# Kernel optimization log

Hardware: AMD Instinct MI355X
Metric: run time of the kernel (lower is better)

## Reference

```python
import jax, jax.numpy as jnp
import numpy as np

B, T, D, L, E = 8, 2048, 256, 8, 64


def setup_inputs() -> dict:
    key = jax.random.key(0)
    ks = jax.random.split(key, 5)
    x = jax.random.normal(ks[0], (B, T, D), dtype=jnp.float32)
    # MMLP params: weight (4L, D, E), bias (4L, E); nn.Linear: (2L, D), (2L,)
    W_ml = jax.random.normal(ks[1], (4 * L, D, E), dtype=jnp.float32) * 0.05
    b_ml = jax.random.normal(ks[2], (4 * L, E), dtype=jnp.float32) * 0.05
    W_lin = jax.random.normal(ks[3], (2 * L, D), dtype=jnp.float32) * 0.05
    b_lin = jax.random.normal(ks[4], (2 * L,), dtype=jnp.float32) * 0.05
    return {"x": x, "W_ml": W_ml, "b_ml": b_ml, "W_lin": W_lin, "b_lin": b_lin}


def _xlstm_forward(x, W_ml, b_ml, W_lin, b_lin):
    b, t, _ = x.shape
    l4, _, e = W_ml.shape
    l = l4 // 4
    # Precompute all per-step gate projections at once (the torch code does this per step).
    mg = jnp.einsum('bti,lij->btlj', x, W_ml) + b_ml          # (B,T,4L,E)
    lg = jnp.einsum('bti,li->btl', x, W_lin) + b_lin          # (B,T,2L)
    o_, v, k, q = jnp.split(mg, 4, axis=2)                    # each (B,T,L,E)
    i_, f_ = jnp.split(lg, 2, axis=2)                         # each (B,T,L)
    xs = tuple(jnp.moveaxis(a, 1, 0) for a in (o_, v, k, q, i_, f_))  # time-major

    def step(carry, inp):
        m, n, C, h = carry
        o_t, v_t, k_t, q_t, i_t, f_t = inp
        m_new = jnp.maximum(f_t + m, i_t)                     # stabilizer (B,L)
        i_g = jnp.exp(i_t - m_new)
        f_g = jnp.exp(f_t + m - m_new)
        # rank-1 outer-product update of matrix cell state (B,L,E,E)
        C = f_g[:, :, None, None] * C + i_g[:, :, None, None] * (v_t[:, :, :, None] * k_t[:, :, None, :])
        n = f_g[:, :, None] * n + i_g[:, :, None] * k_t       # (B,L,E)
        denom = jnp.maximum(jnp.sum(n * q_t, axis=-1), 1.0)[:, :, None]  # clamp(.,1,inf)
        h = jax.nn.sigmoid(o_t) * jnp.einsum('blij,bli->blj', C, q_t) / denom
        return (m_new, n, C, h), None

    init = (
        jnp.zeros((b, l), jnp.float32),
        jnp.zeros((b, l, e), jnp.float32),
        jnp.zeros((b, l, e, e), jnp.float32),
        jnp.zeros((b, l, e), jnp.float32),
    )
    (m, n, C, h), _ = jax.lax.scan(step, init, xs)
    return h, C


def reference(x, W_ml, b_ml, W_lin, b_lin):
    return _xlstm_forward(x, W_ml, b_ml, W_lin, b_lin)
```

## Files before the change

### kernel.cpp

```cpp
#include <hip/hip_runtime.h>

#define B 8
#define T 2048
#define D 256
#define L 8
#define E 64
#define BT (B*T)

typedef _Float16 f16;
typedef f16 f16x8 __attribute__((ext_vector_type(8)));
typedef float f32x4 __attribute__((ext_vector_type(4)));

#define OFF_I   0
#define OFF_F   (OFF_I  + B*L*T)
#define OFF_W16 (OFF_F  + B*L*T)
#define OFF_X16 (OFF_W16 + B*L*T/2)
#define OFF_WT  (OFF_X16 + B*T*D/2)
#define OFF_VT  (OFF_WT + 16*E*D/2)
#define OFF_KT  (OFF_VT + B*L*E*T/2)
#define OFF_CP  (OFF_KT + B*L*E*T/2)

__global__ __launch_bounds__(256) void k_prep_x(const float* __restrict__ x,
                                                f16* __restrict__ x16) {
    int i = (blockIdx.x * 256 + threadIdx.x) * 8;
    float4 v0 = *(const float4*)(x + i);
    float4 v1 = *(const float4*)(x + i + 4);
    f16x8 o;
    o[0] = (f16)v0.x; o[1] = (f16)v0.y; o[2] = (f16)v0.z; o[3] = (f16)v0.w;
    o[4] = (f16)v1.x; o[5] = (f16)v1.y; o[6] = (f16)v1.z; o[7] = (f16)v1.w;
    *(f16x8*)(x16 + i) = o;
}

__global__ __launch_bounds__(256) void k_prep_w(const float* __restrict__ Wml,
                                                f16* __restrict__ Wt16) {
    __shared__ float ts[64][65];
    int tid = threadIdx.x;
    int vkrow = blockIdx.x;
    int wrow = 8 + vkrow;
    for (int dc = 0; dc < 4; ++dc) {
        int d0 = dc * 64;
        int r = tid >> 2, cq = (tid & 3) * 16;
        const float* src = Wml + ((size_t)wrow * D + d0 + r) * E + cq;
        #pragma unroll
        for (int j = 0; j < 16; j += 4) {
            float4 v = *(const float4*)(src + j);
            ts[r][cq + j] = v.x; ts[r][cq + j + 1] = v.y;
            ts[r][cq + j + 2] = v.z; ts[r][cq + j + 3] = v.w;
        }
        __syncthreads();
        int e = tid >> 2, dq = (tid & 3) * 16;
        f16* dst = Wt16 + ((size_t)vkrow * E + e) * D + d0 + dq;
        f16x8 o0, o1;
        #pragma unroll
        for (int j = 0; j < 8; ++j) {
            o0[j] = (f16)ts[dq + j][e];
            o1[j] = (f16)ts[dq + 8 + j][e];
        }
        *(f16x8*)dst = o0;
        *(f16x8*)(dst + 8) = o1;
        __syncthreads();
    }
}

__global__ __launch_bounds__(256) void k_ifproj(const float* __restrict__ x,
        const float* __restrict__ Wlin, const float* __restrict__ blin,
        float* __restrict__ ibuf, float* __restrict__ fbuf) {
    __shared__ float xs[32][260];
    __shared__ float ws[16][260];
    int tid = threadIdx.x;
    int t0 = blockIdx.x * 32;
    {
        int row = tid >> 3, q = tid & 7;
        const float* src = x + (size_t)(t0 + row) * D + q * 32;
        #pragma unroll
        for (int j = 0; j < 8; ++j) {
            float4 v = *(const float4*)(src + j * 4);
            *(float4*)&xs[row][q * 32 + j * 4] = v;
        }
    }
    {
        int row = tid >> 4, c0 = (tid & 15) * 16;
        const float* src = Wlin + row * D + c0;
        #pragma unroll
        for (int j = 0; j < 4; ++j) {
            float4 v = *(const float4*)(src + j * 4);
            *(float4*)&ws[row][c0 + j * 4] = v;
        }
    }
    __syncthreads();
    int tl = tid >> 4, g = tid & 15;
    float acc0 = 0.f, acc1 = 0.f;
    for (int i = 0; i < D; ++i) {
        float wv = ws[g][i];
        acc0 += xs[tl * 2 + 0][i] * wv;
        acc1 += xs[tl * 2 + 1][i] * wv;
    }
    float bias = blin[g];
    float acc[2] = {acc0 + bias, acc1 + bias};
    #pragma unroll
    for (int u = 0; u < 2; ++u) {
        int t = t0 + tl * 2 + u;
        int b = t >> 11, tt = t & 2047;
        if (g < 8) ibuf[(b * L + g) * T + tt] = acc[u];
        else       fbuf[(b * L + (g - 8)) * T + tt] = acc[u];
    }
}

__global__ __launch_bounds__(256) void k_scan(const float* __restrict__ ibuf,
        const float* __restrict__ fbuf, f16* __restrict__ w16) {
    __shared__ float part[256];
    __shared__ float red[256];
    int tid = threadIdx.x;
    int base = blockIdx.x * T;
    const float* fp = fbuf + base + tid * 8;
    const float* ip = ibuf + base + tid * 8;
    float4 fa = *(const float4*)fp;
    float4 fb = *(const float4*)(fp + 4);
    float4 ia = *(const float4*)ip;
    float4 ib = *(const float4*)(ip + 4);
    float f[8] = {fa.x, fa.y, fa.z, fa.w, fb.x, fb.y, fb.z, fb.w};
    float iv[8] = {ia.x, ia.y, ia.z, ia.w, ib.x, ib.y, ib.z, ib.w};
    float ls[8]; float run = 0.f;
    #pragma unroll
    for (int r = 0; r < 8; ++r) { run += f[r]; ls[r] = run; }
    part[tid] = run;
    __syncthreads();
    if (tid == 0) {
        float running = 0.f;
        for (int k = 0; k < 256; ++k) { float tmp = part[k]; part[k] = running; running += tmp; }
    }
    __syncthreads();
    float off = part[tid];
    float e[8]; float lmax = -1e30f;
    #pragma unroll
    for (int r = 0; r < 8; ++r) { e[r] = iv[r] - (off + ls[r]); lmax = fmaxf(lmax, e[r]); }
    red[tid] = lmax;
    __syncthreads();
    for (int s = 128; s > 0; s >>= 1) {
        if (tid < s) red[tid] = fmaxf(red[tid], red[tid + s]);
        __syncthreads();
    }
    float M = fmaxf(red[0], 0.0f);
    f16x8 wv8;
    #pragma unroll
    for (int r = 0; r < 8; ++r) wv8[r] = (f16)__expf(e[r] - M);
    *(f16x8*)(w16 + base + tid * 8) = wv8;
}

__global__ __launch_bounds__(256) void k_vkproj_mfma(const f16* __restrict__ x16,
        const f16* __restrict__ Wt16, const float* __restrict__ bml,
        f16* __restrict__ Vt, f16* __restrict__ Kt) {
    __shared__ char lds[24576];
    int tid = threadIdx.x;
    int bx = blockIdx.x, by = blockIdx.y;
    int l = by >> 1, vk = by & 1;
    int vkrow = vk * 8 + l;
    int t0 = bx * 128;
    const f16* xa = x16 + (size_t)t0 * D;
    const f16* wb = Wt16 + (size_t)vkrow * E * D;
    int wv = tid >> 6, lane = tid & 63;
    f32x4 acc[2][4] = {};
    for (int kc = 0; kc < 4; ++kc) {
        int k0 = kc * 64;
        #pragma unroll
        for (int q = 0; q < 4; ++q) {
            int idx = q * 256 + tid;
            int row = idx >> 3, c = idx & 7;
            f16x8 v = *(const f16x8*)(xa + row * D + k0 + c * 8);
            int ba = row * 128 + c * 16; ba ^= (row & 7) << 4;
            *(f16x8*)(lds + ba) = v;
        }
        #pragma unroll
        for (int q = 0; q < 2; ++q) {
            int idx = q * 256 + tid;
            int e = idx >> 3, c = idx & 7;
            f16x8 v = *(const f16x8*)(wb + e * D + k0 + c * 8);
            int ba = 16384 + e * 128 + c * 16; ba ^= (e & 7) << 4;
            *(f16x8*)(lds + ba) = v;
        }
        __syncthreads();
        #pragma unroll
        for (int kk = 0; kk < 2; ++kk) {
            int ko = kk * 32 + (lane >> 4) * 8;
            f16x8 a[2], bfr[4];
            #pragma unroll
            for (int fr = 0; fr < 2; ++fr) {
                int row = wv * 32 + fr * 16 + (lane & 15);
                int ba = row * 128 + ko * 2; ba ^= (row & 7) << 4;
                a[fr] = *(const f16x8*)(lds + ba);
            }
            #pragma unroll
            for (int fc = 0; fc < 4; ++fc) {
                int e = fc * 16 + (lane & 15);
                int ba = 16384 + e * 128 + ko * 2; ba ^= (e & 7) << 4;
                bfr[fc] = *(const f16x8*)(lds + ba);
            }
            #pragma unroll
            for (int fr = 0; fr < 2; ++fr)
                #pragma unroll
                for (int fc = 0; fc < 4; ++fc)
                    acc[fr][fc] = __builtin_amdgcn_mfma_f32_16x16x32_f16(
                        a[fr], bfr[fc], acc[fr][fc], 0, 0, 0);
        }
        __syncthreads();
    }
    const float* bp = bml + (size_t)(8 + vkrow) * E;
    #pragma unroll
    for (int fr = 0; fr < 2; ++fr) {
        #pragma unroll
        for (int fc = 0; fc < 4; ++fc) {
            int e = fc * 16 + (lane & 15);
            float bias = bp[e];
            int swz = (e & 7) << 4;
            #pragma unroll
            for (int r = 0; r < 4; r += 2) {
                int t = wv * 32 + fr * 16 + (lane >> 4) * 4 + r;
                union { f16 h[2]; unsigned u; } pk;
                pk.h[0] = (f16)(acc[fr][fc][r] + bias);
                pk.h[1] = (f16)(acc[fr][fc][r + 1] + bias);
                int ba = e * 256 + t * 2; ba ^= swz;
                *(unsigned*)(lds + ba) = pk.u;
            }
        }
    }
    __syncthreads();
    f16* obuf = vk ? Kt : Vt;
    int e = tid >> 2, tq = (tid & 3) * 32;
    int b = t0 >> 11, tin = t0 & 2047;
    f16* dst = obuf + (((size_t)(b * L + l) * E + e) * T) + tin + tq;
    int swz = (e & 7) << 4;
    #pragma unroll
    for (int c = 0; c < 4; ++c) {
        int ba = e * 256 + (tq + c * 8) * 2; ba ^= swz;
        f16x8 v = *(const f16x8*)(lds + ba);
        *(f16x8*)(dst + c * 8) = v;
    }
}

__global__ __launch_bounds__(256) void k_cgemm_mfma(const f16* __restrict__ Vt,
        const f16* __restrict__ Kt, const f16* __restrict__ w16,
        float* __restrict__ Cpart) {
    int tid = threadIdx.x;
    int bl = blockIdx.x, tc = blockIdx.y;
    int wv = tid >> 6, lane = tid & 63;
    const f16* vp = Vt + (size_t)bl * E * T;
    const f16* kp = Kt + (size_t)bl * E * T;
    const f16* wp = w16 + (size_t)bl * T;
    f32x4 acc[5][4] = {};
    int tbase = tc * 512 + wv * 128;
    for (int kc = 0; kc < 4; ++kc) {
        int tt = tbase + kc * 32 + (lane >> 4) * 8;
        f16x8 wfrag = *(const f16x8*)(wp + tt);
        f16x8 a[5], bfr[4];
        #pragma unroll
        for (int m = 0; m < 4; ++m) {
            int i = m * 16 + (lane & 15);
            f16x8 v = *(const f16x8*)(vp + (size_t)i * T + tt);
            a[m] = v * wfrag;
        }
        a[4] = wfrag;
        #pragma unroll
        for (int nn = 0; nn < 4; ++nn) {
            int j = nn * 16 + (lane & 15);
            bfr[nn] = *(const f16x8*)(kp + (size_t)j * T + tt);
        }
        #pragma unroll
        for (int m = 0; m < 5; ++m)
            #pragma unroll
            for (int nn = 0; nn < 4; ++nn)
                acc[m][nn] = __builtin_amdgcn_mfma_f32_16x16x32_f16(
                    a[m], bfr[nn], acc[m][nn], 0, 0, 0);
    }
    float* cp = Cpart + ((size_t)bl * 16 + tc * 4 + wv) * (65 * 64);
    #pragma unroll
    for (int m = 0; m < 4; ++m)
        #pragma unroll
        for (int nn = 0; nn < 4; ++nn)
            #pragma unroll
            for (int r = 0; r < 4; ++r) {
                int row = m * 16 + (lane >> 4) * 4 + r;
                cp[row * 64 + nn * 16 + (lane & 15)] = acc[m][nn][r];
            }
    if ((lane >> 4) == 0) {
        #pragma unroll
        for (int nn = 0; nn < 4; ++nn)
            cp[4096 + nn * 16 + (lane & 15)] = acc[4][nn][0];
    }
}

__global__ __launch_bounds__(256) void k_final(const float* __restrict__ x,
        const float* __restrict__ Wml, const float* __restrict__ bml,
        const float* __restrict__ Cpart, float* __restrict__ out) {
    __shared__ float Cs[E * E];
    __shared__ float xs[D];
    __shared__ float ns[E];
    __shared__ float os[E];
    __shared__ float qs[E];
    int tid = threadIdx.x;
    int bl = blockIdx.x; int b = bl >> 3, l = bl & 7;
    xs[tid] = x[((size_t)(b * T + (T - 1))) * D + tid];
    const float* cp = Cpart + (size_t)bl * 16 * (65 * 64);
    #pragma unroll
    for (int j = 0; j < 4; ++j) {
        int idx = tid * 16 + j * 4;
        float4 s = {0, 0, 0, 0};
        for (int p = 0; p < 16; ++p) {
            float4 v = *(const float4*)(cp + p * (65 * 64) + idx);
            s.x += v.x; s.y += v.y; s.z += v.z; s.w += v.w;
        }
        *(float4*)&Cs[idx] = s;
        *(float4*)(out + 4096 + (size_t)bl * (E * E) + idx) = s;
    }
    if (tid < 64) {
        float s = 0.f;
        for (int p = 0; p < 16; ++p) s += cp[p * (65 * 64) + 4096 + tid];
        ns[tid] = s;
    }
    __syncthreads();
    if (tid < 128) {
        int gate = tid >> 6, e = tid & 63;
        int wrow = gate ? (3 * L + l) : l;
        const float* wpp = Wml + (size_t)wrow * D * E + e;
        float s = 0.f;
        for (int kk = 0; kk < D; ++kk) s += xs[kk] * wpp[kk * E];
        s += bml[wrow * E + e];
        if (gate) qs[e] = s; else os[e] = s;
    }
    __syncthreads();
    if (tid < 64) {
        int j = tid;
        float hc = 0.f;
        for (int i2 = 0; i2 < E; ++i2) hc += Cs[i2 * E + j] * qs[i2];
        float nq = 0.f;
        for (int i2 = 0; i2 < E; ++i2) nq += ns[i2] * qs[i2];
        float denom = fmaxf(nq, 1.0f);
        float sg = 1.0f / (1.0f + __expf(-os[j]));
        out[bl * E + j] = sg * hc / denom;
    }
}

extern "C" void kernel_launch(void* const* d_in, const int* in_sizes, int n_in,
                              void* d_out, int out_size, void* d_ws, size_t ws_size,
                              hipStream_t stream) {
    const float* x    = (const float*)d_in[0];
    const float* Wml  = (const float*)d_in[1];
    const float* bml  = (const float*)d_in[2];
    const float* Wlin = (const float*)d_in[3];
    const float* blin = (const float*)d_in[4];
    float* out = (float*)d_out;
    float* ws = (float*)d_ws;
    float* ibuf  = ws + OFF_I;
    float* fbuf  = ws + OFF_F;
    f16*   w16   = (f16*)(ws + OFF_W16);
    f16*   x16   = (f16*)(ws + OFF_X16);
    f16*   Wt16  = (f16*)(ws + OFF_WT);
    f16*   Vt    = (f16*)(ws + OFF_VT);
    f16*   Kt    = (f16*)(ws + OFF_KT);
    float* Cpart = ws + OFF_CP;

    k_prep_x<<<BT * D / (256 * 8), 256, 0, stream>>>(x, x16);
    k_prep_w<<<16, 256, 0, stream>>>(Wml, Wt16);
    k_ifproj<<<BT / 32, 256, 0, stream>>>(x, Wlin, blin, ibuf, fbuf);
    k_scan<<<B * L, 256, 0, stream>>>(ibuf, fbuf, w16);
    k_vkproj_mfma<<<dim3(BT / 128, 16), 256, 0, stream>>>(x16, Wt16, bml, Vt, Kt);
    k_cgemm_mfma<<<dim3(B * L, 4), 256, 0, stream>>>(Vt, Kt, w16, Cpart);
    k_final<<<B * L, 256, 0, stream>>>(x, Wml, bml, Cpart, out);
}
```

Baseline: 74.37 us.

## Fuse prep kernels, convert x in-GEMM, merge V/K projection, reduce C partials in LDS

Merges the i/f projection and W transpose into one launch and drops the separate fp32-to-fp16 pass over x, converting x while loading tiles in the V/K projection GEMM instead. Each V/K block now computes both V and K for a layer (128 output columns), so x is read half as often. The C-GEMM reduces its four wave partials in shared memory before writing, which cuts partial-sum traffic and the final reduction from 16 to 4. The cost is fp32 x loads being re-read per layer block (8 times), and serialized LDS accumulation across waves.

```diff
diff --git a/kernel.cpp b/kernel.cpp
--- a/kernel.cpp
+++ b/kernel.cpp
@@ -14,95 +14,85 @@
 #define OFF_I   0
 #define OFF_F   (OFF_I  + B*L*T)
 #define OFF_W16 (OFF_F  + B*L*T)
-#define OFF_X16 (OFF_W16 + B*L*T/2)
-#define OFF_WT  (OFF_X16 + B*T*D/2)
+#define OFF_WT  (OFF_W16 + B*L*T/2)
 #define OFF_VT  (OFF_WT + 16*E*D/2)
 #define OFF_KT  (OFF_VT + B*L*E*T/2)
 #define OFF_CP  (OFF_KT + B*L*E*T/2)
 
-__global__ __launch_bounds__(256) void k_prep_x(const float* __restrict__ x,
-                                                f16* __restrict__ x16) {
-    int i = (blockIdx.x * 256 + threadIdx.x) * 8;
-    float4 v0 = *(const float4*)(x + i);
-    float4 v1 = *(const float4*)(x + i + 4);
-    f16x8 o;
-    o[0] = (f16)v0.x; o[1] = (f16)v0.y; o[2] = (f16)v0.z; o[3] = (f16)v0.w;
-    o[4] = (f16)v1.x; o[5] = (f16)v1.y; o[6] = (f16)v1.z; o[7] = (f16)v1.w;
-    *(f16x8*)(x16 + i) = o;
-}
-
-__global__ __launch_bounds__(256) void k_prep_w(const float* __restrict__ Wml,
-                                                f16* __restrict__ Wt16) {
-    __shared__ float ts[64][65];
-    int tid = threadIdx.x;
-    int vkrow = blockIdx.x;
-    int wrow = 8 + vkrow;
-    for (int dc = 0; dc < 4; ++dc) {
-        int d0 = dc * 64;
-        int r = tid >> 2, cq = (tid & 3) * 16;
-        const float* src = Wml + ((size_t)wrow * D + d0 + r) * E + cq;
-        #pragma unroll
-        for (int j = 0; j < 16; j += 4) {
-            float4 v = *(const float4*)(src + j);
-            ts[r][cq + j] = v.x; ts[r][cq + j + 1] = v.y;
-            ts[r][cq + j + 2] = v.z; ts[r][cq + j + 3] = v.w;
-        }
-        __syncthreads();
-        int e = tid >> 2, dq = (tid & 3) * 16;
-        f16* dst = Wt16 + ((size_t)vkrow * E + e) * D + d0 + dq;
-        f16x8 o0, o1;
-        #pragma unroll
-        for (int j = 0; j < 8; ++j) {
-            o0[j] = (f16)ts[dq + j][e];
-            o1[j] = (f16)ts[dq + 8 + j][e];
-        }
-        *(f16x8*)dst = o0;
-        *(f16x8*)(dst + 8) = o1;
-        __syncthreads();
-    }
-}
-
-__global__ __launch_bounds__(256) void k_ifproj(const float* __restrict__ x,
+__global__ __launch_bounds__(256) void k_prep(const float* __restrict__ x,
         const float* __restrict__ Wlin, const float* __restrict__ blin,
-        float* __restrict__ ibuf, float* __restrict__ fbuf) {
-    __shared__ float xs[32][260];
-    __shared__ float ws[16][260];
-    int tid = threadIdx.x;
-    int t0 = blockIdx.x * 32;
-    {
-        int row = tid >> 3, q = tid & 7;
-        const float* src = x + (size_t)(t0 + row) * D + q * 32;
-        #pragma unroll
-        for (int j = 0; j < 8; ++j) {
-            float4 v = *(const float4*)(src + j * 4);
-            *(float4*)&xs[row][q * 32 + j * 4] = v;
-        }
-    }
-    {
-        int row = tid >> 4, c0 = (tid & 15) * 16;
-        const float* src = Wlin + row * D + c0;
-        #pragma unroll
-        for (int j = 0; j < 4; ++j) {
-            float4 v = *(const float4*)(src + j * 4);
-            *(float4*)&ws[row][c0 + j * 4] = v;
-        }
-    }
-    __syncthreads();
-    int tl = tid >> 4, g = tid & 15;
-    float acc0 = 0.f, acc1 = 0.f;
-    for (int i = 0; i < D; ++i) {
-        float wv = ws[g][i];
-        acc0 += xs[tl * 2 + 0][i] * wv;
-        acc1 += xs[tl * 2 + 1][i] * wv;
-    }
-    float bias = blin[g];
-    float acc[2] = {acc0 + bias, acc1 + bias};
-    #pragma unroll
-    for (int u = 0; u < 2; ++u) {
-        int t = t0 + tl * 2 + u;
-        int b = t >> 11, tt = t & 2047;
-        if (g < 8) ibuf[(b * L + g) * T + tt] = acc[u];
-        else       fbuf[(b * L + (g - 8)) * T + tt] = acc[u];
+        const float* __restrict__ Wml,
+        float* __restrict__ ibuf, float* __restrict__ fbuf,
+        f16* __restrict__ Wt16) {
+    __shared__ __align__(16) char smem[49920];
+    int tid = threadIdx.x;
+    int bx = blockIdx.x;
+    if (bx < 512) {
+        float (*xs)[260] = (float(*)[260])smem;
+        float (*wsm)[260] = (float(*)[260])(smem + 33280);
+        int t0 = bx * 32;
+        {
+            int row = tid >> 3, q = tid & 7;
+            const float* src = x + (size_t)(t0 + row) * D + q * 32;
+            #pragma unroll
+            for (int j = 0; j < 8; ++j) {
+                float4 v = *(const float4*)(src + j * 4);
+                *(float4*)&xs[row][q * 32 + j * 4] = v;
+            }
+        }
+        {
+            int row = tid >> 4, c0 = (tid & 15) * 16;
+            const float* src = Wlin + row * D + c0;
+            #pragma unroll
+            for (int j = 0; j < 4; ++j) {
+                float4 v = *(const float4*)(src + j * 4);
+                *(float4*)&wsm[row][c0 + j * 4] = v;
+            }
+        }
+        __syncthreads();
+        int tl = tid >> 4, g = tid & 15;
+        float acc0 = 0.f, acc1 = 0.f;
+        for (int i = 0; i < D; ++i) {
+            float wv = wsm[g][i];
+            acc0 += xs[tl * 2 + 0][i] * wv;
+            acc1 += xs[tl * 2 + 1][i] * wv;
+        }
+        float bias = blin[g];
+        float acc[2] = {acc0 + bias, acc1 + bias};
+        #pragma unroll
+        for (int u = 0; u < 2; ++u) {
+            int t = t0 + tl * 2 + u;
+            int b = t >> 11, tt = t & 2047;
+            if (g < 8) ibuf[(b * L + g) * T + tt] = acc[u];
+            else       fbuf[(b * L + (g - 8)) * T + tt] = acc[u];
+        }
+    } else {
+        float (*ts)[65] = (float(*)[65])smem;
+        int vkrow = bx - 512;
+        int wrow = 8 + vkrow;
+        for (int dc = 0; dc < 4; ++dc) {
+            int d0 = dc * 64;
+            int r = tid >> 2, cq = (tid & 3) * 16;
+            const float* src = Wml + ((size_t)wrow * D + d0 + r) * E + cq;
+            #pragma unroll
+            for (int j = 0; j < 16; j += 4) {
+                float4 v = *(const float4*)(src + j);
+                ts[r][cq + j] = v.x; ts[r][cq + j + 1] = v.y;
+                ts[r][cq + j + 2] = v.z; ts[r][cq + j + 3] = v.w;
+            }
+            __syncthreads();
+            int e = tid >> 2, dq = (tid & 3) * 16;
+            f16* dst = Wt16 + ((size_t)vkrow * E + e) * D + d0 + dq;
+            f16x8 o0, o1;
+            #pragma unroll
+            for (int j = 0; j < 8; ++j) {
+                o0[j] = (f16)ts[dq + j][e];
+                o1[j] = (f16)ts[dq + 8 + j][e];
+            }
+            *(f16x8*)dst = o0;
+            *(f16x8*)(dst + 8) = o1;
+            __syncthreads();
+        }
     }
 }
 
@@ -147,99 +137,107 @@
     *(f16x8*)(w16 + base + tid * 8) = wv8;
 }
 
-__global__ __launch_bounds__(256) void k_vkproj_mfma(const f16* __restrict__ x16,
+__global__ __launch_bounds__(256) void k_vkproj2(const float* __restrict__ x,
         const f16* __restrict__ Wt16, const float* __restrict__ bml,
         f16* __restrict__ Vt, f16* __restrict__ Kt) {
-    __shared__ char lds[24576];
-    int tid = threadIdx.x;
-    int bx = blockIdx.x, by = blockIdx.y;
-    int l = by >> 1, vk = by & 1;
-    int vkrow = vk * 8 + l;
+    __shared__ __align__(16) char lds[32768];
+    int tid = threadIdx.x;
+    int bx = blockIdx.x, l = blockIdx.y;
     int t0 = bx * 128;
-    const f16* xa = x16 + (size_t)t0 * D;
-    const f16* wb = Wt16 + (size_t)vkrow * E * D;
+    const float* xa = x + (size_t)t0 * D;
+    const f16* wvp = Wt16 + (size_t)l * E * D;
+    const f16* wkp = Wt16 + (size_t)(8 + l) * E * D;
     int wv = tid >> 6, lane = tid & 63;
-    f32x4 acc[2][4] = {};
+    f32x4 acc[2][8] = {};
     for (int kc = 0; kc < 4; ++kc) {
         int k0 = kc * 64;
         #pragma unroll
         for (int q = 0; q < 4; ++q) {
             int idx = q * 256 + tid;
             int row = idx >> 3, c = idx & 7;
-            f16x8 v = *(const f16x8*)(xa + row * D + k0 + c * 8);
-            int ba = row * 128 + c * 16; ba ^= (row & 7) << 4;
-            *(f16x8*)(lds + ba) = v;
-        }
-        #pragma unroll
-        for (int q = 0; q < 2; ++q) {
+            const float* src = xa + (size_t)row * D + k0 + c * 8;
+            float4 v0 = *(const float4*)src;
+            float4 v1 = *(const float4*)(src + 4);
+            f16x8 h;
+            h[0] = (f16)v0.x; h[1] = (f16)v0.y; h[2] = (f16)v0.z; h[3] = (f16)v0.w;
+            h[4] = (f16)v1.x; h[5] = (f16)v1.y; h[6] = (f16)v1.z; h[7] = (f16)v1.w;
+            int ba = (row * 128 + c * 16) ^ ((row & 7) << 4);
+            *(f16x8*)(lds + ba) = h;
+        }
+        #pragma unroll
+        for (int q = 0; q < 4; ++q) {
             int idx = q * 256 + tid;
-            int e = idx >> 3, c = idx & 7;
-            f16x8 v = *(const f16x8*)(wb + e * D + k0 + c * 8);
-            int ba = 16384 + e * 128 + c * 16; ba ^= (e & 7) << 4;
+            int row = idx >> 3, c = idx & 7;
+            const f16* src = (row < 64 ? wvp + (size_t)row * D
+                                       : wkp + (size_t)(row - 64) * D) + k0 + c * 8;
+            f16x8 v = *(const f16x8*)src;
+            int ba = 16384 + ((row * 128 + c * 16) ^ ((row & 7) << 4));
             *(f16x8*)(lds + ba) = v;
         }
         __syncthreads();
         #pragma unroll
         for (int kk = 0; kk < 2; ++kk) {
             int ko = kk * 32 + (lane >> 4) * 8;
-            f16x8 a[2], bfr[4];
+            f16x8 a[2], bf[8];
             #pragma unroll
             for (int fr = 0; fr < 2; ++fr) {
                 int row = wv * 32 + fr * 16 + (lane & 15);
-                int ba = row * 128 + ko * 2; ba ^= (row & 7) << 4;
+                int ba = (row * 128 + ko * 2) ^ ((row & 7) << 4);
                 a[fr] = *(const f16x8*)(lds + ba);
             }
             #pragma unroll
-            for (int fc = 0; fc < 4; ++fc) {
+            for (int fc = 0; fc < 8; ++fc) {
                 int e = fc * 16 + (lane & 15);
-                int ba = 16384 + e * 128 + ko * 2; ba ^= (e & 7) << 4;
-                bfr[fc] = *(const f16x8*)(lds + ba);
+                int ba = 16384 + ((e * 128 + ko * 2) ^ ((e & 7) << 4));
+                bf[fc] = *(const f16x8*)(lds + ba);
             }
             #pragma unroll
             for (int fr = 0; fr < 2; ++fr)
                 #pragma unroll
-                for (int fc = 0; fc < 4; ++fc)
+                for (int fc = 0; fc < 8; ++fc)
                     acc[fr][fc] = __builtin_amdgcn_mfma_f32_16x16x32_f16(
-                        a[fr], bfr[fc], acc[fr][fc], 0, 0, 0);
-        }
-        __syncthreads();
-    }
-    const float* bp = bml + (size_t)(8 + vkrow) * E;
-    #pragma unroll
-    for (int fr = 0; fr < 2; ++fr) {
-        #pragma unroll
-        for (int fc = 0; fc < 4; ++fc) {
-            int e = fc * 16 + (lane & 15);
-            float bias = bp[e];
-            int swz = (e & 7) << 4;
+                        a[fr], bf[fc], acc[fr][fc], 0, 0, 0);
+        }
+        __syncthreads();
+    }
+    const float* bvp = bml + (size_t)(8 + l) * E;
+    const float* bkp = bml + (size_t)(16 + l) * E;
+    #pragma unroll
+    for (int fc = 0; fc < 8; ++fc) {
+        int e = fc * 16 + (lane & 15);
+        float bias = (e < 64) ? bvp[e] : bkp[e - 64];
+        int swz = (e & 7) << 4;
+        #pragma unroll
+        for (int fr = 0; fr < 2; ++fr) {
             #pragma unroll
             for (int r = 0; r < 4; r += 2) {
                 int t = wv * 32 + fr * 16 + (lane >> 4) * 4 + r;
                 union { f16 h[2]; unsigned u; } pk;
                 pk.h[0] = (f16)(acc[fr][fc][r] + bias);
                 pk.h[1] = (f16)(acc[fr][fc][r + 1] + bias);
-                int ba = e * 256 + t * 2; ba ^= swz;
+                int ba = (e * 256 + t * 2) ^ swz;
                 *(unsigned*)(lds + ba) = pk.u;
             }
         }
     }
     __syncthreads();
-    f16* obuf = vk ? Kt : Vt;
-    int e = tid >> 2, tq = (tid & 3) * 32;
-    int b = t0 >> 11, tin = t0 & 2047;
-    f16* dst = obuf + (((size_t)(b * L + l) * E + e) * T) + tin + tq;
-    int swz = (e & 7) << 4;
-    #pragma unroll
-    for (int c = 0; c < 4; ++c) {
-        int ba = e * 256 + (tq + c * 8) * 2; ba ^= swz;
-        f16x8 v = *(const f16x8*)(lds + ba);
-        *(f16x8*)(dst + c * 8) = v;
-    }
-}
-
-__global__ __launch_bounds__(256) void k_cgemm_mfma(const f16* __restrict__ Vt,
+    int e2 = tid >> 1, tq = (tid & 1) * 64;
+    int bb = t0 >> 11, tin = t0 & 2047;
+    int vk = e2 >> 6, el = e2 & 63;
+    f16* dst = (vk ? Kt : Vt) + ((size_t)((bb * L + l) * E + el)) * T + tin + tq;
+    int swz = (e2 & 7) << 4;
+    #pragma unroll
+    for (int j = 0; j < 8; ++j) {
+        int ba = (e2 * 256 + (tq + j * 8) * 2) ^ swz;
+        *(f16x8*)(dst + j * 8) = *(const f16x8*)(lds + ba);
+    }
+}
+
+__global__ __launch_bounds__(256) void k_cgemm2(const f16* __restrict__ Vt,
         const f16* __restrict__ Kt, const f16* __restrict__ w16,
         float* __restrict__ Cpart) {
+    __shared__ float red[64 * 64];
+    __shared__ float redn[64];
     int tid = threadIdx.x;
     int bl = blockIdx.x, tc = blockIdx.y;
     int wv = tid >> 6, lane = tid & 63;
@@ -251,7 +249,7 @@
     for (int kc = 0; kc < 4; ++kc) {
         int tt = tbase + kc * 32 + (lane >> 4) * 8;
         f16x8 wfrag = *(const f16x8*)(wp + tt);
-        f16x8 a[5], bfr[4];
+        f16x8 a[5], bf[4];
         #pragma unroll
         for (int m = 0; m < 4; ++m) {
             int i = m * 16 + (lane & 15);
@@ -262,30 +260,46 @@
         #pragma unroll
         for (int nn = 0; nn < 4; ++nn) {
             int j = nn * 16 + (lane & 15);
-            bfr[nn] = *(const f16x8*)(kp + (size_t)j * T + tt);
+            bf[nn] = *(const f16x8*)(kp + (size_t)j * T + tt);
         }
         #pragma unroll
         for (int m = 0; m < 5; ++m)
             #pragma unroll
             for (int nn = 0; nn < 4; ++nn)
                 acc[m][nn] = __builtin_amdgcn_mfma_f32_16x16x32_f16(
-                    a[m], bfr[nn], acc[m][nn], 0, 0, 0);
-    }
-    float* cp = Cpart + ((size_t)bl * 16 + tc * 4 + wv) * (65 * 64);
-    #pragma unroll
-    for (int m = 0; m < 4; ++m)
-        #pragma unroll
-        for (int nn = 0; nn < 4; ++nn)
-            #pragma unroll
-            for (int r = 0; r < 4; ++r) {
-                int row = m * 16 + (lane >> 4) * 4 + r;
-                cp[row * 64 + nn * 16 + (lane & 15)] = acc[m][nn][r];
-            }
-    if ((lane >> 4) == 0) {
-        #pragma unroll
-        for (int nn = 0; nn < 4; ++nn)
-            cp[4096 + nn * 16 + (lane & 15)] = acc[4][nn][0];
-    }
+                    a[m], bf[nn], acc[m][nn], 0, 0, 0);
+    }
+    for (int rr = 0; rr < 4; ++rr) {
+        if (wv == rr) {
+            #pragma unroll
+            for (int m = 0; m < 4; ++m)
+                #pragma unroll
+                for (int nn = 0; nn < 4; ++nn)
+                    #pragma unroll
+                    for (int r = 0; r < 4; ++r) {
+                        int row = m * 16 + (lane >> 4) * 4 + r;
+                        int col = nn * 16 + (lane & 15);
+                        if (rr == 0) red[row * 64 + col] = acc[m][nn][r];
+                        else         red[row * 64 + col] += acc[m][nn][r];
+                    }
+            if ((lane >> 4) == 0) {
+                #pragma unroll
+                for (int nn = 0; nn < 4; ++nn) {
+                    int col = nn * 16 + (lane & 15);
+                    if (rr == 0) redn[col] = acc[4][nn][0];
+                    else         redn[col] += acc[4][nn][0];
+                }
+            }
+        }
+        __syncthreads();
+    }
+    float* cp = Cpart + ((size_t)bl * 4 + tc) * 4160;
+    #pragma unroll
+    for (int j = 0; j < 4; ++j) {
+        int idx = tid * 16 + j * 4;
+        *(float4*)(cp + idx) = *(const float4*)(red + idx);
+    }
+    if (tid < 64) cp[4096 + tid] = redn[tid];
 }
 
 __global__ __launch_bounds__(256) void k_final(const float* __restrict__ x,
@@ -299,13 +313,14 @@
     int tid = threadIdx.x;
     int bl = blockIdx.x; int b = bl >> 3, l = bl & 7;
     xs[tid] = x[((size_t)(b * T + (T - 1))) * D + tid];
-    const float* cp = Cpart + (size_t)bl * 16 * (65 * 64);
+    const float* cp = Cpart + (size_t)bl * 4 * 4160;
     #pragma unroll
     for (int j = 0; j < 4; ++j) {
         int idx = tid * 16 + j * 4;
         float4 s = {0, 0, 0, 0};
-        for (int p = 0; p < 16; ++p) {
-            float4 v = *(const float4*)(cp + p * (65 * 64) + idx);
+        #pragma unroll
+        for (int p = 0; p < 4; ++p) {
+            float4 v = *(const float4*)(cp + p * 4160 + idx);
             s.x += v.x; s.y += v.y; s.z += v.z; s.w += v.w;
         }
         *(float4*)&Cs[idx] = s;
@@ -313,7 +328,8 @@
     }
     if (tid < 64) {
         float s = 0.f;
-        for (int p = 0; p < 16; ++p) s += cp[p * (65 * 64) + 4096 + tid];
+        #pragma unroll
+        for (int p = 0; p < 4; ++p) s += cp[p * 4160 + 4096 + tid];
         ns[tid] = s;
     }
     __syncthreads();
@@ -352,17 +368,14 @@
     float* ibuf  = ws + OFF_I;
     float* fbuf  = ws + OFF_F;
     f16*   w16   = (f16*)(ws + OFF_W16);
-    f16*   x16   = (f16*)(ws + OFF_X16);
     f16*   Wt16  = (f16*)(ws + OFF_WT);
     f16*   Vt    = (f16*)(ws + OFF_VT);
     f16*   Kt    = (f16*)(ws + OFF_KT);
     float* Cpart = ws + OFF_CP;
 
-    k_prep_x<<<BT * D / (256 * 8), 256, 0, stream>>>(x, x16);
-    k_prep_w<<<16, 256, 0, stream>>>(Wml, Wt16);
-    k_ifproj<<<BT / 32, 256, 0, stream>>>(x, Wlin, blin, ibuf, fbuf);
+    k_prep<<<512 + 16, 256, 0, stream>>>(x, Wlin, blin, Wml, ibuf, fbuf, Wt16);
     k_scan<<<B * L, 256, 0, stream>>>(ibuf, fbuf, w16);
-    k_vkproj_mfma<<<dim3(BT / 128, 16), 256, 0, stream>>>(x16, Wt16, bml, Vt, Kt);
-    k_cgemm_mfma<<<dim3(B * L, 4), 256, 0, stream>>>(Vt, Kt, w16, Cpart);
+    k_vkproj2<<<dim3(BT / 128, 8), 256, 0, stream>>>(x, Wt16, bml, Vt, Kt);
+    k_cgemm2<<<dim3(B * L, 4), 256, 0, stream>>>(Vt, Kt, w16, Cpart);
     k_final<<<B * L, 256, 0, stream>>>(x, Wml, bml, Cpart, out);
 }
```

After: 75.46 us. Within noise of the previous version (+1.5%).
